# Optimization experiments

Hardware: AMD Instinct MI355X
Metric: run time of the kernel (lower is better)

The kernel has to match this reference:

```python
import jax, jax.numpy as jnp
import numpy as np


def setup_inputs() -> dict:
    key = jax.random.key(0)
    k1, k2, k3 = jax.random.split(key, 3)
    B, S, D, H = 16, 2048, 1024, 1024
    inp = jax.random.normal(k1, (B, S, D), dtype=jnp.float32)
    W = jax.random.normal(k2, (3 * H, D), dtype=jnp.float32) * (1.0 / np.sqrt(D))
    b = jax.random.normal(k3, (3 * H,), dtype=jnp.float32) * 0.01
    return {"inp": inp, "W": W, "b": b}


def _forget_mult(z, f):
    # z, f: [B, S, H]; h_t = f_t*z_t + (1-f_t)*h_{t-1}, h_{-1}=0 (hid=None)
    zT = jnp.swapaxes(z, 0, 1)  # [S, B, H]
    fT = jnp.swapaxes(f, 0, 1)

    def step(h, zf):
        z_t, f_t = zf
        h = f_t * z_t + (1.0 - f_t) * h
        return h, h

    h0 = jnp.zeros_like(zT[0])
    _, cT = jax.lax.scan(step, h0, (zT, fT))
    return jnp.swapaxes(cT, 0, 1)  # [B, S, H]


def reference(inp, W, b):
    # window=1, batch_first=True, output_gate=True, backward=False, hid=None
    y = jnp.einsum('bsd,hd->bsh', inp, W) + b  # [B, S, 3H]
    z_gate, f_gate, o_gate = jnp.split(y, 3, axis=2)
    z_gate = jnp.tanh(z_gate)
    f_gate = jax.nn.sigmoid(f_gate)
    c_gate = _forget_mult(z_gate, f_gate)
    output = jax.nn.sigmoid(o_gate) * c_gate
    return output, c_gate[:, -1]
```

## Files before the change

### kernel.cpp

```cpp
#include <hip/hip_runtime.h>


typedef unsigned short ushort_t;
typedef __bf16 bf16x8 __attribute__((ext_vector_type(8)));
typedef float f32x4 __attribute__((ext_vector_type(4)));
typedef ushort_t us8 __attribute__((ext_vector_type(8)));

__device__ __forceinline__ ushort_t f2bf(float f) {
  unsigned int x = __builtin_bit_cast(unsigned int, f);
  x += 0x7fffu + ((x >> 16) & 1u);
  return (ushort_t)(x >> 16);
}
__device__ __forceinline__ float bf2f(ushort_t u) {
  unsigned int x = ((unsigned int)u) << 16;
  return __builtin_bit_cast(float, x);
}
__device__ __forceinline__ float loadg(const float* p) { return *p; }
__device__ __forceinline__ float loadg(const ushort_t* p) { return bf2f(*p); }
__device__ __forceinline__ void storeg(float* p, float v) { *p = v; }
__device__ __forceinline__ void storeg(ushort_t* p, float v) { *p = f2bf(v); }

__device__ __forceinline__ float sig_f(float x) { return 1.0f / (1.0f + __expf(-x)); }
__device__ __forceinline__ float tanh_f(float x) { return 1.0f - 2.0f / (1.0f + __expf(2.0f * x)); }

__device__ __forceinline__ void gload_lds16(const ushort_t* g, ushort_t* l) {
  __builtin_amdgcn_global_load_lds(
      (const __attribute__((address_space(1))) void*)g,
      (__attribute__((address_space(3))) void*)l, 16, 0, 0);
}

__global__ void __launch_bounds__(256) cvt_f32_bf16(
    const float* __restrict__ in, ushort_t* __restrict__ out, long n8) {
  long i = (long)blockIdx.x * 256 + threadIdx.x;
  const long stride = (long)gridDim.x * 256;
  for (; i < n8; i += stride) {
    const float4 a = ((const float4*)in)[2 * i];
    const float4 c = ((const float4*)in)[2 * i + 1];
    us8 w;
    w[0] = f2bf(a.x); w[1] = f2bf(a.y); w[2] = f2bf(a.z); w[3] = f2bf(a.w);
    w[4] = f2bf(c.x); w[5] = f2bf(c.y); w[6] = f2bf(c.z); w[7] = f2bf(c.w);
    ((us8*)out)[i] = w;
  }
}

template <typename GT>
__global__ void __launch_bounds__(256) gemm_gates(
    const ushort_t* __restrict__ A, const ushort_t* __restrict__ Wt,
    const float* __restrict__ bias, GT* __restrict__ out,
    int M, int N, int K) {
  constexpr int BK = 64;
  __shared__ __align__(16) ushort_t As[128 * BK];
  __shared__ __align__(16) ushort_t Bs[128 * BK];
  const int tid = threadIdx.x;
  const int lane = tid & 63;
  const int wv = tid >> 6;
  const int nblk = N >> 7;
  const int bn = blockIdx.x % nblk;
  const int bm = blockIdx.x / nblk;
  const int m0 = bm << 7, n0 = bn << 7;
  const int wm = (wv >> 1) << 6, wn = (wv & 1) << 6;

  f32x4 acc[4][4] = {};

  const int srow = lane >> 3;
  const int sg = (lane & 7) ^ srow;

  for (int kt = 0; kt < K; kt += BK) {
    __syncthreads();
#pragma unroll
    for (int i = 0; i < 4; ++i) {
      const int rbase = wv * 32 + i * 8;
      gload_lds16(&A[(size_t)(m0 + rbase + srow) * K + kt + sg * 8],
                  &As[rbase * 64]);
      gload_lds16(&Wt[(size_t)(n0 + rbase + srow) * K + kt + sg * 8],
                  &Bs[rbase * 64]);
    }
    __syncthreads();
#pragma unroll
    for (int ks = 0; ks < 2; ++ks) {
      bf16x8 af[4], bfr[4];
#pragma unroll
      for (int t = 0; t < 4; ++t) {
        const int ar = wm + t * 16 + (lane & 15);
        const int ag = ((ks << 2) + (lane >> 4)) ^ (ar & 7);
        af[t] = *(const bf16x8*)&As[ar * 64 + ag * 8];
        const int br = wn + t * 16 + (lane & 15);
        const int bg = ((ks << 2) + (lane >> 4)) ^ (br & 7);
        bfr[t] = *(const bf16x8*)&Bs[br * 64 + bg * 8];
      }
#pragma unroll
      for (int i = 0; i < 4; ++i)
#pragma unroll
        for (int j = 0; j < 4; ++j)
          acc[i][j] =
              __builtin_amdgcn_mfma_f32_16x16x32_bf16(af[i], bfr[j], acc[i][j], 0, 0, 0);
    }
  }

  const int gcat = n0 >> 10;
  const int cn = lane & 15;
  const int cm = (lane >> 4) << 2;
#pragma unroll
  for (int j = 0; j < 4; ++j) {
    const int n = n0 + wn + j * 16 + cn;
    const float bv = bias[n];
#pragma unroll
    for (int i = 0; i < 4; ++i) {
#pragma unroll
      for (int r = 0; r < 4; ++r) {
        const int m = m0 + wm + i * 16 + cm + r;
        const float y = acc[i][j][r] + bv;
        const float v = (gcat == 0) ? tanh_f(y) : sig_f(y);
        storeg(&out[(size_t)m * N + n], v);
      }
    }
  }
}

template <typename GT>
__global__ void __launch_bounds__(256) qrnn_chunk_agg(
    const GT* __restrict__ gates, float* __restrict__ aggG,
    float* __restrict__ aggA, int b0, int S, int H, int C, int L) {
  const int nhb = H >> 8;
  const int hb = blockIdx.x % nhb;
  const int c = (blockIdx.x / nhb) % C;
  const int bl = blockIdx.x / (nhb * C);
  const int h = (hb << 8) + threadIdx.x;
  const int N3 = 3 * H;
  const GT* pz = gates + ((size_t)(bl * S + c * L)) * N3 + h;
  const GT* pf = pz + H;
  float G = 1.0f, Aa = 0.0f;
#pragma unroll 4
  for (int j = 0; j < L; ++j) {
    const float z = loadg(pz);
    const float f = loadg(pf);
    const float g = 1.0f - f;
    Aa = fmaf(g, Aa, f * z);
    G *= g;
    pz += N3;
    pf += N3;
  }
  const size_t idx = ((size_t)((b0 + bl) * C + c)) * H + h;
  aggG[idx] = G;
  aggA[idx] = Aa;
}

template <typename GT>
__global__ void __launch_bounds__(256) qrnn_scan_apply(
    const GT* __restrict__ gates, const float* __restrict__ aggG,
    const float* __restrict__ aggA, float* __restrict__ out,
    int b0, int B, int S, int H, int C, int L) {
  const int nhb = H >> 8;
  const int hb = blockIdx.x % nhb;
  const int c = (blockIdx.x / nhb) % C;
  const int bl = blockIdx.x / (nhb * C);
  const int bg = b0 + bl;
  const int h = (hb << 8) + threadIdx.x;
  const int N3 = 3 * H;

  float hc = 0.0f;
  for (int cc = 0; cc < c; ++cc) {
    const size_t idx = ((size_t)(bg * C + cc)) * H + h;
    hc = fmaf(aggG[idx], hc, aggA[idx]);
  }

  const GT* pz = gates + ((size_t)(bl * S + c * L)) * N3 + h;
  const GT* pf = pz + H;
  const GT* po = pf + H;
  size_t oidx = ((size_t)(bg * S + c * L)) * H + h;
#pragma unroll 4
  for (int j = 0; j < L; ++j) {
    const float z = loadg(pz);
    const float f = loadg(pf);
    const float o = loadg(po);
    hc = fmaf(1.0f - f, hc, f * z);
    out[oidx] = o * hc;
    pz += N3; pf += N3; po += N3; oidx += H;
  }
  if (c == C - 1) {
    out[(size_t)B * S * H + (size_t)bg * H + h] = hc;
  }
}

template <typename GT>
static void run_groups(const float* inp, const ushort_t* Wbf, const float* b,
                       float* out, ushort_t* Abf, void* gates_ws, float* aggG,
                       float* aggA, int Bg, int B, int S, int H, int K, int C,
                       int L, hipStream_t stream) {
  const int N = 3 * H;
  GT* gates = (GT*)gates_ws;
  for (int b0 = 0; b0 < B; b0 += Bg) {
    const int Mg = Bg * S;
    const long n8 = (long)Mg * K / 8;
    const long cg = (n8 + 255) / 256;
    const int cgrid = (int)(cg < 2048 ? cg : 2048);
    cvt_f32_bf16<<<cgrid, 256, 0, stream>>>(inp + (size_t)b0 * S * K, Abf, n8);
    const int gemm_grid = (Mg / 128) * (N / 128);
    const int scan_grid = Bg * C * (H / 256);
    gemm_gates<GT><<<gemm_grid, 256, 0, stream>>>(Abf, Wbf, b, gates, Mg, N, K);
    qrnn_chunk_agg<GT><<<scan_grid, 256, 0, stream>>>(
        gates, aggG, aggA, b0, S, H, C, L);
    qrnn_scan_apply<GT><<<scan_grid, 256, 0, stream>>>(
        gates, aggG, aggA, out, b0, B, S, H, C, L);
  }
}

extern "C" void kernel_launch(void* const* d_in, const int* in_sizes, int n_in,
                              void* d_out, int out_size, void* d_ws, size_t ws_size,
                              hipStream_t stream) {
  (void)in_sizes; (void)n_in; (void)out_size;
  const float* inp = (const float*)d_in[0];
  const float* W = (const float*)d_in[1];
  const float* b = (const float*)d_in[2];
  float* out = (float*)d_out;

  constexpr int B = 16, S = 2048, H = 1024, K = 1024;
  constexpr int C = 16, L = S / C;
  const int N3 = 3 * H;

  const size_t agg_elems = (size_t)B * C * H;
  float* aggG = (float*)d_ws;
  float* aggA = aggG + agg_elems;
  ushort_t* Wbf = (ushort_t*)(aggA + agg_elems);
  ushort_t* Abf = Wbf + (size_t)N3 * K;
  const size_t hdr =
      2 * agg_elems * sizeof(float) + (size_t)N3 * K * sizeof(ushort_t);

  int Bg = 0;
  bool f32g = true;
  for (int g = 16; g >= 1; g >>= 1) {
    const size_t need =
        hdr + (size_t)g * S * K * sizeof(ushort_t) + (size_t)g * S * N3 * sizeof(float);
    if (need <= ws_size) { Bg = g; break; }
  }
  if (!Bg) {
    f32g = false;
    for (int g = 16; g >= 1; g >>= 1) {
      const size_t need = hdr + (size_t)g * S * K * sizeof(ushort_t) +
                          (size_t)g * S * N3 * sizeof(ushort_t);
      if (need <= ws_size) { Bg = g; break; }
    }
  }
  if (!Bg) return;
  void* gates_ws = (void*)(Abf + (size_t)Bg * S * K);

  {
    const long n8w = (long)N3 * K / 8;
    const long cg = (n8w + 255) / 256;
    const int grid = (int)(cg < 2048 ? cg : 2048);
    cvt_f32_bf16<<<grid, 256, 0, stream>>>(W, Wbf, n8w);
  }

  if (f32g) {
    run_groups<float>(inp, Wbf, b, out, Abf, gates_ws, aggG, aggA, Bg,
                      B, S, H, K, C, L, stream);
  } else {
    run_groups<ushort_t>(inp, Wbf, b, out, Abf, gates_ws, aggG, aggA, Bg,
                         B, S, H, K, C, L, stream);
  }
}
```

Baseline: 712.9 us.

## Vectorize scan kernels by four, raise chunk count, remap GEMM blocks per XCD

The chunked scan kernels now handle four hidden units per thread with 128-bit (or 64-bit for bf16) loads and stores instead of scalar accesses. The chunk count rises from 16 to 64 so the grid keeps enough blocks after the fourfold cut in blocks per chunk. The GEMM also remaps block IDs so that consecutive tiles land on the same XCD, aiming for better L2 reuse. The larger chunk count lengthens the serial carry-in loop in the apply kernel and enlarges the aggregate workspace.

```diff
diff --git a/kernel.cpp b/kernel.cpp
--- a/kernel.cpp
+++ b/kernel.cpp
@@ -15,10 +15,24 @@
   unsigned int x = ((unsigned int)u) << 16;
   return __builtin_bit_cast(float, x);
 }
-__device__ __forceinline__ float loadg(const float* p) { return *p; }
-__device__ __forceinline__ float loadg(const ushort_t* p) { return bf2f(*p); }
 __device__ __forceinline__ void storeg(float* p, float v) { *p = v; }
 __device__ __forceinline__ void storeg(ushort_t* p, float v) { *p = f2bf(v); }
+
+__device__ __forceinline__ f32x4 loadg4(const float* p) {
+  return *(const f32x4*)p;
+}
+__device__ __forceinline__ f32x4 loadg4(const ushort_t* p) {
+  ushort4 u = *(const ushort4*)p;
+  f32x4 r;
+  r[0] = bf2f(u.x); r[1] = bf2f(u.y); r[2] = bf2f(u.z); r[3] = bf2f(u.w);
+  return r;
+}
+__device__ __forceinline__ f32x4 fma4(f32x4 a, f32x4 b, f32x4 c) {
+  f32x4 r;
+#pragma unroll
+  for (int k = 0; k < 4; ++k) r[k] = fmaf(a[k], b[k], c[k]);
+  return r;
+}
 
 __device__ __forceinline__ float sig_f(float x) { return 1.0f / (1.0f + __expf(-x)); }
 __device__ __forceinline__ float tanh_f(float x) { return 1.0f - 2.0f / (1.0f + __expf(2.0f * x)); }
@@ -54,9 +68,16 @@
   const int tid = threadIdx.x;
   const int lane = tid & 63;
   const int wv = tid >> 6;
+
+  const int nwg = gridDim.x;
+  const int bid0 = blockIdx.x;
+  const int q = nwg >> 3, r = nwg & 7;
+  const int xcd = bid0 & 7, loc = bid0 >> 3;
+  const int bid = (xcd < r ? xcd * (q + 1) : r * (q + 1) + (xcd - r) * q) + loc;
+
   const int nblk = N >> 7;
-  const int bn = blockIdx.x % nblk;
-  const int bm = blockIdx.x / nblk;
+  const int bn = bid % nblk;
+  const int bm = bid / nblk;
   const int m0 = bm << 7, n0 = bn << 7;
   const int wm = (wv >> 1) << 6, wn = (wv & 1) << 6;
 
@@ -121,28 +142,29 @@
 __global__ void __launch_bounds__(256) qrnn_chunk_agg(
     const GT* __restrict__ gates, float* __restrict__ aggG,
     float* __restrict__ aggA, int b0, int S, int H, int C, int L) {
-  const int nhb = H >> 8;
+  const int nhb = H >> 10;
   const int hb = blockIdx.x % nhb;
   const int c = (blockIdx.x / nhb) % C;
   const int bl = blockIdx.x / (nhb * C);
-  const int h = (hb << 8) + threadIdx.x;
+  const int h = (hb << 10) + threadIdx.x * 4;
   const int N3 = 3 * H;
   const GT* pz = gates + ((size_t)(bl * S + c * L)) * N3 + h;
   const GT* pf = pz + H;
-  float G = 1.0f, Aa = 0.0f;
+  f32x4 G = {1.0f, 1.0f, 1.0f, 1.0f};
+  f32x4 Aa = {0.0f, 0.0f, 0.0f, 0.0f};
 #pragma unroll 4
   for (int j = 0; j < L; ++j) {
-    const float z = loadg(pz);
-    const float f = loadg(pf);
-    const float g = 1.0f - f;
-    Aa = fmaf(g, Aa, f * z);
+    const f32x4 z = loadg4(pz);
+    const f32x4 f = loadg4(pf);
+    const f32x4 g = 1.0f - f;
+    Aa = fma4(g, Aa, f * z);
     G *= g;
     pz += N3;
     pf += N3;
   }
   const size_t idx = ((size_t)((b0 + bl) * C + c)) * H + h;
-  aggG[idx] = G;
-  aggA[idx] = Aa;
+  *(f32x4*)&aggG[idx] = G;
+  *(f32x4*)&aggA[idx] = Aa;
 }
 
 template <typename GT>
@@ -150,18 +172,18 @@
     const GT* __restrict__ gates, const float* __restrict__ aggG,
     const float* __restrict__ aggA, float* __restrict__ out,
     int b0, int B, int S, int H, int C, int L) {
-  const int nhb = H >> 8;
+  const int nhb = H >> 10;
   const int hb = blockIdx.x % nhb;
   const int c = (blockIdx.x / nhb) % C;
   const int bl = blockIdx.x / (nhb * C);
   const int bg = b0 + bl;
-  const int h = (hb << 8) + threadIdx.x;
+  const int h = (hb << 10) + threadIdx.x * 4;
   const int N3 = 3 * H;
 
-  float hc = 0.0f;
+  f32x4 hc = {0.0f, 0.0f, 0.0f, 0.0f};
   for (int cc = 0; cc < c; ++cc) {
     const size_t idx = ((size_t)(bg * C + cc)) * H + h;
-    hc = fmaf(aggG[idx], hc, aggA[idx]);
+    hc = fma4(*(const f32x4*)&aggG[idx], hc, *(const f32x4*)&aggA[idx]);
   }
 
   const GT* pz = gates + ((size_t)(bl * S + c * L)) * N3 + h;
@@ -170,15 +192,15 @@
   size_t oidx = ((size_t)(bg * S + c * L)) * H + h;
 #pragma unroll 4
   for (int j = 0; j < L; ++j) {
-    const float z = loadg(pz);
-    const float f = loadg(pf);
-    const float o = loadg(po);
-    hc = fmaf(1.0f - f, hc, f * z);
-    out[oidx] = o * hc;
+    const f32x4 z = loadg4(pz);
+    const f32x4 f = loadg4(pf);
+    const f32x4 o = loadg4(po);
+    hc = fma4(1.0f - f, hc, f * z);
+    *(f32x4*)&out[oidx] = o * hc;
     pz += N3; pf += N3; po += N3; oidx += H;
   }
   if (c == C - 1) {
-    out[(size_t)B * S * H + (size_t)bg * H + h] = hc;
+    *(f32x4*)&out[(size_t)B * S * H + (size_t)bg * H + h] = hc;
   }
 }
 
@@ -196,7 +218,7 @@
     const int cgrid = (int)(cg < 2048 ? cg : 2048);
     cvt_f32_bf16<<<cgrid, 256, 0, stream>>>(inp + (size_t)b0 * S * K, Abf, n8);
     const int gemm_grid = (Mg / 128) * (N / 128);
-    const int scan_grid = Bg * C * (H / 256);
+    const int scan_grid = Bg * C * (H / 1024);
     gemm_gates<GT><<<gemm_grid, 256, 0, stream>>>(Abf, Wbf, b, gates, Mg, N, K);
     qrnn_chunk_agg<GT><<<scan_grid, 256, 0, stream>>>(
         gates, aggG, aggA, b0, S, H, C, L);
@@ -215,7 +237,7 @@
   float* out = (float*)d_out;
 
   constexpr int B = 16, S = 2048, H = 1024, K = 1024;
-  constexpr int C = 16, L = S / C;
+  constexpr int C = 64, L = S / C;
   const int N3 = 3 * H;
 
   const size_t agg_elems = (size_t)B * C * H;
```

After: 740.1 us. 1.04x slower.
